# Kernel optimization log

Measured on AMD Instinct MI355X. Metric: run time of the kernel, lower is better.

## Reference

```python
import jax, jax.numpy as jnp
import numpy as np

B, T, C = 2, 2048, 1024
NUM_HEADS, QK_LEN, V_LEN = 16, 64, 64


def setup_inputs() -> dict:
    key = jax.random.key(0)
    ks = jax.random.split(key, 11)
    s = 0.02
    return {
        "Q": jax.random.normal(ks[0], (B, T, C), jnp.float32),
        "K": jax.random.normal(ks[1], (B, T, C), jnp.float32),
        "V": jax.random.normal(ks[2], (B, T, C), jnp.float32),
        # Linear weights stored as (in, out); y = x @ W + b
        "Wq": jax.random.normal(ks[3], (C, NUM_HEADS * QK_LEN), jnp.float32) * s,
        "bq": jnp.zeros((NUM_HEADS * QK_LEN,), jnp.float32),
        "Wk": jax.random.normal(ks[4], (C, NUM_HEADS * QK_LEN), jnp.float32) * s,
        "bk": jnp.zeros((NUM_HEADS * QK_LEN,), jnp.float32),
        "Wv": jax.random.normal(ks[5], (C, NUM_HEADS * V_LEN), jnp.float32) * s,
        "bv": jnp.zeros((NUM_HEADS * V_LEN,), jnp.float32),
        "Wo": jax.random.normal(ks[6], (NUM_HEADS * V_LEN, C), jnp.float32) * s,
        "bo": jnp.zeros((C,), jnp.float32),
    }


def _split_heads(x, n_heads, d):
    b, t, _ = x.shape
    return x.reshape(b, t, n_heads, d).transpose(0, 2, 1, 3)  # (B,H,T,d)


def reference(Q, K, V, Wq, bq, Wk, bk, Wv, bv, Wo, bo):
    q = _split_heads(Q @ Wq + bq, NUM_HEADS, QK_LEN)   # (B,H,T,dk)
    k = _split_heads(K @ Wk + bk, NUM_HEADS, QK_LEN)   # (B,H,T,dk)
    v = _split_heads(V @ Wv + bv, NUM_HEADS, V_LEN)    # (B,H,T,dv)

    scale = 1.0 / jnp.sqrt(jnp.asarray(QK_LEN, q.dtype))
    scores = jnp.einsum("bhqd,bhkd->bhqk", q, k) * scale  # (B,H,T,T)
    attn = jax.nn.softmax(scores, axis=-1)
    out = jnp.einsum("bhqk,bhkd->bhqd", attn, v)           # (B,H,T,dv)

    out = out.transpose(0, 2, 1, 3).reshape(Q.shape[0], Q.shape[1], NUM_HEADS * V_LEN)
    return out @ Wo + bo
```

## Files before the change

kernel.cpp:

```cpp
#include <hip/hip_runtime.h>
#include <hip/hip_bf16.h>
#include <math.h>

constexpr int B = 2, T = 2048, C = 1024, H = 16, D = 64;
constexpr int M = B * T;
constexpr float SCALE_L2E = 0.125f * 1.4426950408889634f;

typedef __attribute__((ext_vector_type(8))) short s16x8;
typedef __attribute__((ext_vector_type(4))) short s16x4;
typedef __attribute__((ext_vector_type(4))) float fv4;

typedef unsigned short ushort_t;

static __device__ __forceinline__ ushort_t f2bf(float x) {
    union { float f; unsigned u; } c; c.f = x;
    unsigned u = c.u + 0x7FFFu + ((c.u >> 16) & 1u);
    return (ushort_t)(u >> 16);
}

static __device__ __forceinline__ int cvt_pk_bf16(float lo, float hi) {
    int r;
    asm("v_cvt_pk_bf16_f32 %0, %1, %2" : "=v"(r) : "v"(lo), "v"(hi));
    return r;
}

#define GLDS(gp, lp) __builtin_amdgcn_global_load_lds( \
    (const __attribute__((address_space(1))) void*)(gp), \
    (__attribute__((address_space(3))) void*)(lp), 16, 0, 0)

__global__ __launch_bounds__(256) void prep(
    const float* __restrict__ Q, const float* __restrict__ K,
    const float* __restrict__ V,
    const float* __restrict__ W0, const float* __restrict__ W1,
    const float* __restrict__ W2, const float* __restrict__ W3,
    ushort_t* __restrict__ dst, ushort_t* __restrict__ Wt)
{
    __shared__ ushort_t tile[64][72];
    const int tid = threadIdx.x;

    if (blockIdx.x < 6144) {
        size_t e = ((size_t)blockIdx.x * 256 + tid) * 8;
        const float* src;
        size_t base;
        if (e < (size_t)M * C)          { src = Q; base = 0; }
        else if (e < 2 * (size_t)M * C) { src = K; base = (size_t)M * C; }
        else                            { src = V; base = 2 * (size_t)M * C; }
        const float* p = src + (e - base);
        float4 a = *(const float4*)p;
        float4 b = *(const float4*)(p + 4);
        union { s16x8 v; int i[4]; } o;
        o.i[0] = cvt_pk_bf16(a.x, a.y);
        o.i[1] = cvt_pk_bf16(a.z, a.w);
        o.i[2] = cvt_pk_bf16(b.x, b.y);
        o.i[3] = cvt_pk_bf16(b.z, b.w);
        *(s16x8*)(dst + e) = o.v;
        return;
    }

    const int idx = blockIdx.x - 6144;
    const int s = idx >> 8;
    const float* W = (s == 0) ? W0 : (s == 1) ? W1 : (s == 2) ? W2 : W3;
    const int k0 = (idx & 15) * 64, n0 = ((idx >> 4) & 15) * 64;
#pragma unroll
    for (int it = 0; it < 4; it++) {
        int f = it * 256 + tid;
        int r = f >> 4, c4 = (f & 15) * 4;
        float4 x = *(const float4*)(W + (size_t)(k0 + r) * C + n0 + c4);
        *(int*)&tile[r][c4]     = cvt_pk_bf16(x.x, x.y);
        *(int*)&tile[r][c4 + 2] = cvt_pk_bf16(x.z, x.w);
    }
    __syncthreads();
#pragma unroll
    for (int it = 0; it < 4; it++) {
        int f = it * 256 + tid;
        int rr = f >> 4, c4 = (f & 15) * 4;
        union { s16x4 v; ushort_t u[4]; } u;
#pragma unroll
        for (int j = 0; j < 4; j++) u.u[j] = tile[c4 + j][rr];
        *(s16x4*)(Wt + (size_t)(s * 1024 + n0 + rr) * 1024 + k0 + c4) = u.v;
    }
}

__global__ __launch_bounds__(256) void gemm_qkv(
    const ushort_t* __restrict__ qkv, const ushort_t* __restrict__ Wt,
    const float* __restrict__ bq, const float* __restrict__ bk,
    const float* __restrict__ bv,
    ushort_t* __restrict__ qw, ushort_t* __restrict__ kw,
    ushort_t* __restrict__ vt)
{
    __shared__ alignas(16) ushort_t sm[17408];
    ushort_t* As0 = sm;
    ushort_t* Bs0 = sm + 8192;

    const int tid = threadIdx.x;
    const int w = tid >> 6, lane = tid & 63;
    const int quad = lane >> 4, lc = lane & 15;
    const int wm = w & 1, wn = w >> 1;

    const int lin = blockIdx.y * 24 + blockIdx.x;
    const int xcd = lin % 8;
    const int i_ = lin / 8;
    const int s = i_ >> 5;
    const int r_ = i_ & 31;
    const int m0 = (xcd * 4 + (r_ >> 3)) * 128;
    const int nt = s * 8 + (r_ & 7);
    const int nsec0 = (nt & 7) * 128;

    const ushort_t* Abase = qkv + (size_t)s * M * C;
    const ushort_t* Btbase = Wt + (size_t)nt * 128 * 1024;

    const int srow = (w << 4) + (lane >> 2);
    const int ske  = (lane & 3) * 8;

    fv4 acc[4][4] = {};

    auto stage = [&](int k0, int buf) {
#pragma unroll
        for (int i = 0; i < 2; i++) {
            int row = i * 64 + srow;
            GLDS(Abase + (size_t)(m0 + row) * 1024 + k0 + ske,
                 As0 + buf * 4096 + i * 2048 + w * 512);
            GLDS(Btbase + (size_t)row * 1024 + k0 + ske,
                 Bs0 + buf * 4096 + i * 2048 + w * 512);
        }
    };

    stage(0, 0);
    __syncthreads();

    for (int k0 = 0; k0 < 1024; k0 += 32) {
        const int cur = (k0 >> 5) & 1;
        if (k0 + 32 < 1024) stage(k0 + 32, cur ^ 1);

        s16x8 af[4], bf[4];
#pragma unroll
        for (int ms = 0; ms < 4; ms++)
            af[ms] = *(const s16x8*)(As0 + cur * 4096 + (wm * 64 + ms * 16 + lc) * 32 + quad * 8);
#pragma unroll
        for (int ns = 0; ns < 4; ns++)
            bf[ns] = *(const s16x8*)(Bs0 + cur * 4096 + (wn * 64 + ns * 16 + lc) * 32 + quad * 8);
#pragma unroll
        for (int ms = 0; ms < 4; ms++)
#pragma unroll
            for (int ns = 0; ns < 4; ns++)
                acc[ms][ns] = __builtin_amdgcn_mfma_f32_16x16x32_bf16(
                    af[ms], bf[ns], acc[ms][ns], 0, 0, 0);
        __syncthreads();
    }

    if (s == 2) {
        ushort_t* tp = sm;
#pragma unroll
        for (int ns = 0; ns < 4; ns++) {
            const int nl = wn * 64 + ns * 16 + lc;
            const float bias = bv[nsec0 + nl];
#pragma unroll
            for (int ms = 0; ms < 4; ms++) {
                const int ml = wm * 64 + ms * 16 + quad * 4;
                union { s16x4 v; int i2[2]; } u;
                u.i2[0] = cvt_pk_bf16(acc[ms][ns][0] + bias, acc[ms][ns][1] + bias);
                u.i2[1] = cvt_pk_bf16(acc[ms][ns][2] + bias, acc[ms][ns][3] + bias);
                *(s16x4*)&tp[nl * 136 + ml] = u.v;
            }
        }
        __syncthreads();
        const int b_ = m0 >> 11, t0 = m0 & 2047;
#pragma unroll
        for (int it = 0; it < 8; it++) {
            const int row = it * 16 + (tid >> 4);
            const int ch = tid & 15;
            const int n = nsec0 + row;
            const int h_ = n >> 6, d_ = n & 63;
            s16x8 v8 = *(const s16x8*)&tp[row * 136 + ch * 8];
            *(s16x8*)(vt + ((size_t)(b_ * H + h_) * 64 + d_) * T + t0 + ch * 8) = v8;
        }
        return;
    }

    const float* biasp = (s == 0) ? bq : bk;
    const float premul = (s == 0) ? SCALE_L2E : 1.0f;
    ushort_t* outp = (s == 0) ? qw : kw;

#pragma unroll
    for (int ns = 0; ns < 4; ns++) {
        const int nl = nsec0 + wn * 64 + ns * 16 + lc;
        const float bias = biasp[nl];
        const int h_ = nl >> 6, d_ = nl & 63;
#pragma unroll
        for (int ms = 0; ms < 4; ms++) {
#pragma unroll
            for (int r = 0; r < 4; r++) {
                int m = m0 + wm * 64 + ms * 16 + quad * 4 + r;
                float val = (acc[ms][ns][r] + bias) * premul;
                int b_ = m >> 11, t_ = m & (T - 1);
                size_t bh = (size_t)(b_ * H + h_);
                outp[((bh * T + t_) << 6) + d_] = f2bf(val);
            }
        }
    }
}

__global__ __launch_bounds__(256) void gemm_final(
    const ushort_t* __restrict__ A, const ushort_t* __restrict__ Wot,
    const float* __restrict__ bo, float* __restrict__ out)
{
    __shared__ alignas(16) ushort_t As[2][128 * 64];
    __shared__ alignas(16) ushort_t Bs[2][64 * 64];

    const int tid = threadIdx.x;
    const int w = tid >> 6, lane = tid & 63;
    const int quad = lane >> 4, lc = lane & 15;
    const int wm = w & 1, wn = w >> 1;
    const int c7 = lc & 7;

    const int lin = blockIdx.y * 16 + blockIdx.x;
    const int xcd = lin & 7;
    const int i_ = lin >> 3;
    const int m0 = (xcd * 4 + (i_ >> 4)) * 128;
    const int n0 = (i_ & 15) * 64;

    const int r8 = lane >> 3;
    const int sch = (lane & 7) ^ r8;

    fv4 acc[4][2] = {};

    auto stage = [&](int k0, int buf) {
#pragma unroll
        for (int i = 0; i < 4; i++) {
            int row = w * 32 + i * 8 + r8;
            GLDS(A + (size_t)(m0 + row) * 1024 + k0 + sch * 8,
                 As[buf] + (w * 32 + i * 8) * 64);
        }
#pragma unroll
        for (int i = 0; i < 2; i++) {
            int row = w * 16 + i * 8 + r8;
            GLDS(Wot + (size_t)(n0 + row) * 1024 + k0 + sch * 8,
                 Bs[buf] + (w * 16 + i * 8) * 64);
        }
    };

    stage(0, 0);
    __syncthreads();

    for (int k0 = 0; k0 < 1024; k0 += 64) {
        const int cur = (k0 >> 6) & 1;
        if (k0 + 64 < 1024) stage(k0 + 64, cur ^ 1);

        s16x8 af[4][2], bf[2][2];
#pragma unroll
        for (int ms = 0; ms < 4; ms++) {
            const int row = wm * 64 + ms * 16 + lc;
#pragma unroll
            for (int kh = 0; kh < 2; kh++)
                af[ms][kh] = *(const s16x8*)(As[cur] + row * 64
                                             + (((kh * 4 + quad) ^ c7) << 3));
        }
#pragma unroll
        for (int ns = 0; ns < 2; ns++) {
            const int row = wn * 32 + ns * 16 + lc;
#pragma unroll
            for (int kh = 0; kh < 2; kh++)
                bf[ns][kh] = *(const s16x8*)(Bs[cur] + row * 64
                                             + (((kh * 4 + quad) ^ c7) << 3));
        }
#pragma unroll
        for (int ms = 0; ms < 4; ms++)
#pragma unroll
            for (int ns = 0; ns < 2; ns++)
#pragma unroll
                for (int kh = 0; kh < 2; kh++)
                    acc[ms][ns] = __builtin_amdgcn_mfma_f32_16x16x32_bf16(
                        af[ms][kh], bf[ns][kh], acc[ms][ns], 0, 0, 0);
        __syncthreads();
    }

#pragma unroll
    for (int ns = 0; ns < 2; ns++) {
        const int n = n0 + wn * 32 + ns * 16 + lc;
        const float bias = bo[n];
#pragma unroll
        for (int ms = 0; ms < 4; ms++) {
#pragma unroll
            for (int r = 0; r < 4; r++) {
                int m = m0 + wm * 64 + ms * 16 + quad * 4 + r;
                out[(size_t)m * 1024 + n] = acc[ms][ns][r] + bias;
            }
        }
    }
}

__global__ __launch_bounds__(256, 4) void attn(
    const ushort_t* __restrict__ q, const ushort_t* __restrict__ k,
    const ushort_t* __restrict__ vT, ushort_t* __restrict__ o)
{
    __shared__ alignas(16) ushort_t ks[2][64 * 64];
    __shared__ alignas(16) ushort_t vs[2][64 * 64];

    const int tid = threadIdx.x;
    const int w = tid >> 6, lane = tid & 63;
    const int quad = lane >> 4, lc = lane & 15;
    const int cs = lc & 7;
    const int qsub = w & 1, ksub = w >> 1;

    const int id = blockIdx.y * 32 + blockIdx.x;
    const int qt = (id >> 3) & 31;
    const int bh = (id & 7) * 4 + (id >> 8);

    s16x8 aq[2][2];
    const ushort_t* qb = q + ((size_t)bh * T + qt * 64 + qsub * 32) * D;
#pragma unroll
    for (int j = 0; j < 2; j++)
#pragma unroll
        for (int h = 0; h < 2; h++)
            aq[j][h] = *(const s16x8*)(qb + (size_t)(j * 16 + lc) * D + h * 32 + quad * 8);

    union { s16x8 v; ushort_t u[8]; } ones;
#pragma unroll
    for (int i = 0; i < 8; i++) ones.u[i] = 0x3F80;

    fv4 accO[2][4] = {};
    fv4 accPS[2] = {};

    const ushort_t* kb0 = k + (size_t)bh * T * D;
    const ushort_t* vb0 = vT + (size_t)bh * D * T;

    const int sr8 = lane >> 3;
    const int sch = (lane & 7) ^ sr8;

    auto stage = [&](int kt, int buf) {
#pragma unroll
        for (int i = 0; i < 2; i++) {
            const int r = w * 16 + i * 8 + sr8;
            GLDS(kb0 + (size_t)(kt * 64 + r) * 64 + sch * 8,
                 ks[buf] + (w * 16 + i * 8) * 64);
            GLDS(vb0 + (size_t)r * T + kt * 64 + sch * 8,
                 vs[buf] + (w * 16 + i * 8) * 64);
        }
    };

    stage(0, 0);

    for (int kt = 0; kt < T / 64; kt++) {
        const int cur = kt & 1;
        if (kt + 1 < T / 64) {
            stage(kt + 1, cur ^ 1);
            asm volatile("s_waitcnt vmcnt(4)" ::: "memory");
        } else {
            asm volatile("s_waitcnt vmcnt(0)" ::: "memory");
        }
        __builtin_amdgcn_s_barrier();
        __builtin_amdgcn_sched_barrier(0);

        fv4 accST[2][2] = {};
        __builtin_amdgcn_s_setprio(1);
#pragma unroll
        for (int t4k = 0; t4k < 2; t4k++) {
            const int row = ksub * 32 + t4k * 16 + lc;
            s16x8 ak0 = *(const s16x8*)(ks[cur] + row * 64 + ((quad ^ cs) << 3));
            s16x8 ak1 = *(const s16x8*)(ks[cur] + row * 64 + (((quad + 4) ^ cs) << 3));
#pragma unroll
            for (int j = 0; j < 2; j++) {
                accST[j][t4k] = __builtin_amdgcn_mfma_f32_16x16x32_bf16(
                    ak0, aq[j][0], accST[j][t4k], 0, 0, 0);
                accST[j][t4k] = __builtin_amdgcn_mfma_f32_16x16x32_bf16(
                    ak1, aq[j][1], accST[j][t4k], 0, 0, 0);
            }
        }
        __builtin_amdgcn_s_setprio(0);

        s16x8 av[4];
#pragma unroll
        for (int t4v = 0; t4v < 4; t4v++) {
            const int row = t4v * 16 + lc;
            av[t4v] = *(const s16x8*)(vs[cur] + row * 64 + (((ksub * 4 + quad) ^ cs) << 3));
        }

#pragma unroll
        for (int j = 0; j < 2; j++) {
            float p0 = __builtin_amdgcn_exp2f(accST[j][0][0]);
            float p1 = __builtin_amdgcn_exp2f(accST[j][0][1]);
            float p2 = __builtin_amdgcn_exp2f(accST[j][0][2]);
            float p3 = __builtin_amdgcn_exp2f(accST[j][0][3]);
            float p4 = __builtin_amdgcn_exp2f(accST[j][1][0]);
            float p5 = __builtin_amdgcn_exp2f(accST[j][1][1]);
            float p6 = __builtin_amdgcn_exp2f(accST[j][1][2]);
            float p7 = __builtin_amdgcn_exp2f(accST[j][1][3]);

            int W00 = cvt_pk_bf16(p0, p1);
            int W01 = cvt_pk_bf16(p2, p3);
            int W10 = cvt_pk_bf16(p4, p5);
            int W11 = cvt_pk_bf16(p6, p7);
            asm("v_permlane32_swap_b32 %0, %1" : "+v"(W00), "+v"(W10));
            asm("v_permlane16_swap_b32 %0, %1" : "+v"(W00), "+v"(W10));
            asm("v_permlane32_swap_b32 %0, %1" : "+v"(W01), "+v"(W11));
            asm("v_permlane16_swap_b32 %0, %1" : "+v"(W01), "+v"(W11));

            union { int i[4]; s16x8 v; } pbu;
            pbu.i[0] = W00; pbu.i[1] = W01; pbu.i[2] = W10; pbu.i[3] = W11;

            __builtin_amdgcn_s_setprio(1);
#pragma unroll
            for (int t4v = 0; t4v < 4; t4v++)
                accO[j][t4v] = __builtin_amdgcn_mfma_f32_16x16x32_bf16(
                    av[t4v], pbu.v, accO[j][t4v], 0, 0, 0);
            accPS[j] = __builtin_amdgcn_mfma_f32_16x16x32_bf16(
                ones.v, pbu.v, accPS[j], 0, 0, 0);
            __builtin_amdgcn_s_setprio(0);
        }

        __builtin_amdgcn_s_barrier();
    }

    float psum[2] = { accPS[0][0], accPS[1][0] };

    float* sc = (float*)&ks[0][0];
#pragma unroll
    for (int c = 0; c < 4; c++) {
        const int j = c >> 1, tv = (c & 1) * 2;
        __syncthreads();
        if (ksub == 1) {
            *(fv4*)(sc + ((qsub * 64 + lane) * 8))     = accO[j][tv];
            *(fv4*)(sc + ((qsub * 64 + lane) * 8 + 4)) = accO[j][tv + 1];
        }
        __syncthreads();
        if (ksub == 0) {
            accO[j][tv]     += *(fv4*)(sc + ((qsub * 64 + lane) * 8));
            accO[j][tv + 1] += *(fv4*)(sc + ((qsub * 64 + lane) * 8 + 4));
        }
    }
    __syncthreads();
    if (ksub == 1) {
        sc[(qsub * 64 + lane) * 2]     = psum[0];
        sc[(qsub * 64 + lane) * 2 + 1] = psum[1];
    }
    __syncthreads();
    if (ksub == 0) {
        psum[0] += sc[(qsub * 64 + lane) * 2];
        psum[1] += sc[(qsub * 64 + lane) * 2 + 1];

        const int b_ = bh >> 4, h_ = bh & 15;
#pragma unroll
        for (int j = 0; j < 2; j++) {
            float inv = 1.0f / psum[j];
            int row = qt * 64 + qsub * 32 + j * 16 + lc;
            ushort_t* op = o + ((size_t)b_ * T + row) * C + h_ * 64;
#pragma unroll
            for (int t4v = 0; t4v < 4; t4v++) {
                union { s16x4 v; int i[2]; } u;
                u.i[0] = cvt_pk_bf16(accO[j][t4v][0] * inv, accO[j][t4v][1] * inv);
                u.i[1] = cvt_pk_bf16(accO[j][t4v][2] * inv, accO[j][t4v][3] * inv);
                *(s16x4*)(op + t4v * 16 + quad * 4) = u.v;
            }
        }
    }
}

extern "C" void kernel_launch(void* const* d_in, const int* in_sizes, int n_in,
                              void* d_out, int out_size, void* d_ws, size_t ws_size,
                              hipStream_t stream)
{
    const float* Q  = (const float*)d_in[0];
    const float* K  = (const float*)d_in[1];
    const float* V  = (const float*)d_in[2];
    const float* Wq = (const float*)d_in[3];
    const float* bq = (const float*)d_in[4];
    const float* Wk = (const float*)d_in[5];
    const float* bk = (const float*)d_in[6];
    const float* Wv = (const float*)d_in[7];
    const float* bv = (const float*)d_in[8];
    const float* Wo = (const float*)d_in[9];
    const float* bo = (const float*)d_in[10];
    float* out = (float*)d_out;

    ushort_t* qkvbf = (ushort_t*)d_ws;
    ushort_t* Wt = qkvbf + (size_t)3 * M * C;
    ushort_t* qw = Wt + (size_t)4096 * 1024;
    ushort_t* kw = qw + (size_t)M * C;
    ushort_t* vt = kw + (size_t)M * C;
    ushort_t* ow = qkvbf;
    ushort_t* Wot = Wt + (size_t)3072 * 1024;

    dim3 blk(256);
    prep<<<dim3(7168), blk, 0, stream>>>(Q, K, V, Wq, Wk, Wv, Wo, qkvbf, Wt);
    gemm_qkv<<<dim3(24, 32), blk, 0, stream>>>(qkvbf, Wt, bq, bk, bv, qw, kw, vt);
    attn<<<dim3(T / 64, B * H), blk, 0, stream>>>(qw, kw, vt, ow);
    gemm_final<<<dim3(16, 32), blk, 0, stream>>>(ow, Wot, bo, out);
}
```

Baseline: 215.7 us.

## Fuse fp32-to-bf16 activation conversion into QKV GEMM and relax loop barriers

Drops the separate pass that converts Q/K/V from fp32 to bf16. The QKV GEMM now streams fp32 activations straight into swizzled LDS and converts them to bf16 when building MFMA fragments. This removes one full read and write of the activations. Both GEMM main loops also swap __syncthreads for explicit vmcnt waits plus raw s_barrier, so prefetched tiles can stay in flight across iterations. In exchange, the QKV GEMM reads twice the bytes for A, uses more LDS, and each A tile is converted once per block that reads it (8 N-tiles), rather than once overall.

Measured after the change: 219.8 us. Within noise of the previous version (+1.9%).

```diff
diff --git a/kernel.cpp b/kernel.cpp
--- a/kernel.cpp
+++ b/kernel.cpp
@@ -29,35 +29,13 @@
     (__attribute__((address_space(3))) void*)(lp), 16, 0, 0)
 
 __global__ __launch_bounds__(256) void prep(
-    const float* __restrict__ Q, const float* __restrict__ K,
-    const float* __restrict__ V,
     const float* __restrict__ W0, const float* __restrict__ W1,
     const float* __restrict__ W2, const float* __restrict__ W3,
-    ushort_t* __restrict__ dst, ushort_t* __restrict__ Wt)
+    ushort_t* __restrict__ Wt)
 {
     __shared__ ushort_t tile[64][72];
     const int tid = threadIdx.x;
-
-    if (blockIdx.x < 6144) {
-        size_t e = ((size_t)blockIdx.x * 256 + tid) * 8;
-        const float* src;
-        size_t base;
-        if (e < (size_t)M * C)          { src = Q; base = 0; }
-        else if (e < 2 * (size_t)M * C) { src = K; base = (size_t)M * C; }
-        else                            { src = V; base = 2 * (size_t)M * C; }
-        const float* p = src + (e - base);
-        float4 a = *(const float4*)p;
-        float4 b = *(const float4*)(p + 4);
-        union { s16x8 v; int i[4]; } o;
-        o.i[0] = cvt_pk_bf16(a.x, a.y);
-        o.i[1] = cvt_pk_bf16(a.z, a.w);
-        o.i[2] = cvt_pk_bf16(b.x, b.y);
-        o.i[3] = cvt_pk_bf16(b.z, b.w);
-        *(s16x8*)(dst + e) = o.v;
-        return;
-    }
-
-    const int idx = blockIdx.x - 6144;
+    const int idx = blockIdx.x;
     const int s = idx >> 8;
     const float* W = (s == 0) ? W0 : (s == 1) ? W1 : (s == 2) ? W2 : W3;
     const int k0 = (idx & 15) * 64, n0 = ((idx >> 4) & 15) * 64;
@@ -82,20 +60,22 @@
 }
 
 __global__ __launch_bounds__(256) void gemm_qkv(
-    const ushort_t* __restrict__ qkv, const ushort_t* __restrict__ Wt,
+    const float* __restrict__ Qf, const float* __restrict__ Kf,
+    const float* __restrict__ Vf, const ushort_t* __restrict__ Wt,
     const float* __restrict__ bq, const float* __restrict__ bk,
     const float* __restrict__ bv,
     ushort_t* __restrict__ qw, ushort_t* __restrict__ kw,
     ushort_t* __restrict__ vt)
 {
-    __shared__ alignas(16) ushort_t sm[17408];
-    ushort_t* As0 = sm;
-    ushort_t* Bs0 = sm + 8192;
+    __shared__ alignas(16) ushort_t sm[24576];
+    float* Asf = (float*)sm;
+    ushort_t* Bs0 = sm + 16384;
 
     const int tid = threadIdx.x;
     const int w = tid >> 6, lane = tid & 63;
     const int quad = lane >> 4, lc = lane & 15;
     const int wm = w & 1, wn = w >> 1;
+    const int c7 = lc & 7;
 
     const int lin = blockIdx.y * 24 + blockIdx.x;
     const int xcd = lin % 8;
@@ -106,36 +86,60 @@
     const int nt = s * 8 + (r_ & 7);
     const int nsec0 = (nt & 7) * 128;
 
-    const ushort_t* Abase = qkv + (size_t)s * M * C;
+    const float* Af = (s == 0) ? Qf : (s == 1) ? Kf : Vf;
     const ushort_t* Btbase = Wt + (size_t)nt * 128 * 1024;
 
     const int srow = (w << 4) + (lane >> 2);
     const int ske  = (lane & 3) * 8;
 
+    const int r8 = lane >> 3;
+    const int sca = ((lane & 7) ^ r8) * 4;
+
     fv4 acc[4][4] = {};
 
     auto stage = [&](int k0, int buf) {
+#pragma unroll
+        for (int i = 0; i < 4; i++) {
+            int row = w * 32 + i * 8 + r8;
+            GLDS(Af + (size_t)(m0 + row) * 1024 + k0 + sca,
+                 Asf + buf * 4096 + (w * 32 + i * 8) * 32);
+        }
 #pragma unroll
         for (int i = 0; i < 2; i++) {
             int row = i * 64 + srow;
-            GLDS(Abase + (size_t)(m0 + row) * 1024 + k0 + ske,
-                 As0 + buf * 4096 + i * 2048 + w * 512);
             GLDS(Btbase + (size_t)row * 1024 + k0 + ske,
                  Bs0 + buf * 4096 + i * 2048 + w * 512);
         }
     };
 
     stage(0, 0);
-    __syncthreads();
-
-    for (int k0 = 0; k0 < 1024; k0 += 32) {
-        const int cur = (k0 >> 5) & 1;
-        if (k0 + 32 < 1024) stage(k0 + 32, cur ^ 1);
+
+    for (int kt = 0; kt < 32; kt++) {
+        const int cur = kt & 1;
+        const int k0 = kt * 32;
+        if (kt + 1 < 32) {
+            stage(k0 + 32, cur ^ 1);
+            asm volatile("s_waitcnt vmcnt(6)" ::: "memory");
+        } else {
+            asm volatile("s_waitcnt vmcnt(0)" ::: "memory");
+        }
+        __builtin_amdgcn_s_barrier();
+        __builtin_amdgcn_sched_barrier(0);
 
         s16x8 af[4], bf[4];
 #pragma unroll
-        for (int ms = 0; ms < 4; ms++)
-            af[ms] = *(const s16x8*)(As0 + cur * 4096 + (wm * 64 + ms * 16 + lc) * 32 + quad * 8);
+        for (int ms = 0; ms < 4; ms++) {
+            const int row = wm * 64 + ms * 16 + lc;
+            const float* ap = Asf + cur * 4096 + row * 32;
+            fv4 x0 = *(const fv4*)(ap + ((( 2 * quad)     ^ c7) << 2));
+            fv4 x1 = *(const fv4*)(ap + ((( 2 * quad + 1) ^ c7) << 2));
+            union { s16x8 v; int i2[4]; } u;
+            u.i2[0] = cvt_pk_bf16(x0[0], x0[1]);
+            u.i2[1] = cvt_pk_bf16(x0[2], x0[3]);
+            u.i2[2] = cvt_pk_bf16(x1[0], x1[1]);
+            u.i2[3] = cvt_pk_bf16(x1[2], x1[3]);
+            af[ms] = u.v;
+        }
 #pragma unroll
         for (int ns = 0; ns < 4; ns++)
             bf[ns] = *(const s16x8*)(Bs0 + cur * 4096 + (wn * 64 + ns * 16 + lc) * 32 + quad * 8);
@@ -145,7 +149,7 @@
             for (int ns = 0; ns < 4; ns++)
                 acc[ms][ns] = __builtin_amdgcn_mfma_f32_16x16x32_bf16(
                     af[ms], bf[ns], acc[ms][ns], 0, 0, 0);
-        __syncthreads();
+        __builtin_amdgcn_s_barrier();
     }
 
     if (s == 2) {
@@ -240,11 +244,18 @@
     };
 
     stage(0, 0);
-    __syncthreads();
-
-    for (int k0 = 0; k0 < 1024; k0 += 64) {
-        const int cur = (k0 >> 6) & 1;
-        if (k0 + 64 < 1024) stage(k0 + 64, cur ^ 1);
+
+    for (int kt = 0; kt < 16; kt++) {
+        const int cur = kt & 1;
+        const int k0 = kt * 64;
+        if (kt + 1 < 16) {
+            stage(k0 + 64, cur ^ 1);
+            asm volatile("s_waitcnt vmcnt(6)" ::: "memory");
+        } else {
+            asm volatile("s_waitcnt vmcnt(0)" ::: "memory");
+        }
+        __builtin_amdgcn_s_barrier();
+        __builtin_amdgcn_sched_barrier(0);
 
         s16x8 af[4][2], bf[2][2];
 #pragma unroll
@@ -271,7 +282,7 @@
                 for (int kh = 0; kh < 2; kh++)
                     acc[ms][ns] = __builtin_amdgcn_mfma_f32_16x16x32_bf16(
                         af[ms][kh], bf[ns][kh], acc[ms][ns], 0, 0, 0);
-        __syncthreads();
+        __builtin_amdgcn_s_barrier();
     }
 
 #pragma unroll
@@ -472,17 +483,16 @@
     const float* bo = (const float*)d_in[10];
     float* out = (float*)d_out;
 
-    ushort_t* qkvbf = (ushort_t*)d_ws;
-    ushort_t* Wt = qkvbf + (size_t)3 * M * C;
+    ushort_t* ow = (ushort_t*)d_ws;
+    ushort_t* Wt = ow + (size_t)3 * M * C;
     ushort_t* qw = Wt + (size_t)4096 * 1024;
     ushort_t* kw = qw + (size_t)M * C;
     ushort_t* vt = kw + (size_t)M * C;
-    ushort_t* ow = qkvbf;
     ushort_t* Wot = Wt + (size_t)3072 * 1024;
 
     dim3 blk(256);
-    prep<<<dim3(7168), blk, 0, stream>>>(Q, K, V, Wq, Wk, Wv, Wo, qkvbf, Wt);
-    gemm_qkv<<<dim3(24, 32), blk, 0, stream>>>(qkvbf, Wt, bq, bk, bv, qw, kw, vt);
+    prep<<<dim3(1024), blk, 0, stream>>>(Wq, Wk, Wv, Wo, Wt);
+    gemm_qkv<<<dim3(24, 32), blk, 0, stream>>>(Q, K, V, Wt, bq, bk, bv, qw, kw, vt);
     attn<<<dim3(T / 64, B * H), blk, 0, stream>>>(qw, kw, vt, ow);
     gemm_final<<<dim3(16, 32), blk, 0, stream>>>(ow, Wot, bo, out);
 }
```
